# Kernel optimization log

Hardware: AMD Instinct MI355X
Metric: run time of the kernel (lower is better)

The kernel has to match this reference:

```python
import jax, jax.numpy as jnp
import numpy as np
from jax import lax

DIM = 64
HEADS = 4
B, Q, V = 8, 128, 128


def _modrelu(z, b):
    m = jnp.abs(z)
    return z * (jax.nn.relu(m + b) / (m + 1e-5))


def _eunn_unitary(h, th1, ph1, th2, ph2, om):
    # tunable-style EUNN, capacity 2: even-pair rotations, odd-pair rotations, diagonal phase
    d = h.shape[-1]
    # layer 1: pairs (0,1),(2,3),...
    hp = h.reshape(*h.shape[:-1], d // 2, 2)
    a, b = hp[..., 0], hp[..., 1]
    c1, s1, e1 = jnp.cos(th1), jnp.sin(th1), jnp.exp(1j * ph1)
    h = jnp.stack([e1 * (c1 * a - s1 * b), s1 * a + c1 * b], -1).reshape(h.shape)
    # layer 2: pairs (1,2),(3,4),...,(d-3,d-2); endpoints pass through
    mid = h[..., 1:d - 1].reshape(*h.shape[:-1], d // 2 - 1, 2)
    a, b = mid[..., 0], mid[..., 1]
    c2, s2, e2 = jnp.cos(th2), jnp.sin(th2), jnp.exp(1j * ph2)
    mid2 = jnp.stack([e2 * (c2 * a - s2 * b), s2 * a + c2 * b], -1).reshape(*h.shape[:-1], d - 2)
    h = jnp.concatenate([h[..., :1], mid2, h[..., d - 1:]], -1)
    return h * jnp.exp(1j * om)


def _forward(queries, values, U_re, U_im, bias, theta1, phi1, theta2, phi2, omega, W_dense, b_dense):
    Bq, Qq, d = queries.shape
    Vv = values.shape[1]
    # quadratic (query, value) expansion -> [B*Q, V, 2d]
    dq = jnp.broadcast_to(queries[:, :, None, :], (Bq, Qq, Vv, d))
    dv = jnp.broadcast_to(values[:, None, :, :], (Bq, Qq, Vv, d))
    x = jnp.concatenate([dq, dv], -1).reshape(Bq * Qq, Vv, 2 * d)
    U = (U_re + 1j * U_im)  # [H, 2d, d] complex input kernel per head
    Ux = jnp.einsum('nvi,hij->hvnj', x.astype(jnp.complex64), U)  # [H, V, N, d]

    def run_head(Ux_h, t1, p1, t2, p2, om, bh):
        def step(h, u):
            h2 = _modrelu(_eunn_unitary(h, t1, p1, t2, p2, om) + u, bh)
            return h2, None
        h0 = jnp.zeros(Ux_h.shape[1:], dtype=jnp.complex64)  # [N, d]
        hT, _ = lax.scan(step, h0, Ux_h)
        return hT  # final state, as Keras RNN with return_sequences=False

    outs = jax.vmap(run_head)(Ux, theta1, phi1, theta2, phi2, omega, bias)  # [H, N, d]
    acc = jnp.real(outs).transpose(1, 0, 2).reshape(Bq * Qq, HEADS * d)
    y = acc @ W_dense + b_dense
    return y.reshape(Bq, Qq, d)


def setup_inputs() -> dict:
    key = jax.random.key(0)
    ks = jax.random.split(key, 12)
    pi = np.pi
    return {
        'queries': jax.random.normal(ks[0], (B, Q, DIM), jnp.float32),
        'values': jax.random.normal(ks[1], (B, V, DIM), jnp.float32),
        'U_re': jax.random.normal(ks[2], (HEADS, 2 * DIM, DIM), jnp.float32) * (1.0 / np.sqrt(2 * DIM)),
        'U_im': jax.random.normal(ks[3], (HEADS, 2 * DIM, DIM), jnp.float32) * (1.0 / np.sqrt(2 * DIM)),
        'bias': jax.random.normal(ks[4], (HEADS, DIM), jnp.float32) * 0.01,
        'theta1': jax.random.uniform(ks[5], (HEADS, DIM // 2), jnp.float32, -pi, pi),
        'phi1': jax.random.uniform(ks[6], (HEADS, DIM // 2), jnp.float32, -pi, pi),
        'theta2': jax.random.uniform(ks[7], (HEADS, DIM // 2 - 1), jnp.float32, -pi, pi),
        'phi2': jax.random.uniform(ks[8], (HEADS, DIM // 2 - 1), jnp.float32, -pi, pi),
        'omega': jax.random.uniform(ks[9], (HEADS, DIM), jnp.float32, -pi, pi),
        'W_dense': jax.random.normal(ks[10], (HEADS * DIM, DIM), jnp.float32) * (1.0 / np.sqrt(HEADS * DIM)),
        'b_dense': jnp.zeros((DIM,), jnp.float32),
    }


def reference(queries, values, U_re, U_im, bias, theta1, phi1, theta2, phi2, omega, W_dense, b_dense):
    return _forward(queries, values, U_re, U_im, bias, theta1, phi1, theta2, phi2, omega, W_dense, b_dense)
```

## Files before the change

kernel.cpp:

```cpp
#include <hip/hip_runtime.h>
#include <math.h>

#define DIM 64
#define HEADS 4
#define BB 8
#define QQ 128
#define VV 128
#define NN (BB*QQ)

typedef float f2 __attribute__((ext_vector_type(2)));

template <int CTRL>
__device__ __forceinline__ float dppf(float x) {
    return __int_as_float(__builtin_amdgcn_update_dpp(
        0, __float_as_int(x), CTRL, 0xF, 0xF, true));
}
#define SWAP1 0xB1
#define WSHR1 0x138
#define WSHL1 0x130

__global__ __launch_bounds__(256) void k_av(const float* __restrict__ values,
                                            const float* __restrict__ U_re,
                                            const float* __restrict__ U_im,
                                            f2* __restrict__ Av) {
    int tid = blockIdx.x * blockDim.x + threadIdx.x;
    int w = tid >> 6;
    int j = tid & 63;
    int h = w >> 9;
    int r0 = (w & 511) << 1;
    const float* vrow = values + r0 * DIM;
    const float* ur = U_re + (h * 2 * DIM + DIM) * DIM + j;
    const float* ui = U_im + (h * 2 * DIM + DIM) * DIM + j;
    f2 a0 = 0.f, a1 = 0.f;
    #pragma unroll 8
    for (int i = 0; i < DIM; ++i) {
        f2 u; u.x = ur[i * DIM]; u.y = ui[i * DIM];
        a0 += vrow[i] * u;
        a1 += vrow[DIM + i] * u;
    }
    f2* out = Av + (h * 1024 + r0) * DIM + j;
    out[0] = a0; out[DIM] = a1;
}

__global__ __launch_bounds__(256, 4) void k_rnn_dense(
        const float* __restrict__ queries,
        const float* __restrict__ U_re,
        const float* __restrict__ U_im,
        const float* __restrict__ bias,
        const float* __restrict__ theta1,
        const float* __restrict__ phi1,
        const float* __restrict__ theta2,
        const float* __restrict__ phi2,
        const float* __restrict__ omega,
        const f2* __restrict__ Av,
        const float* __restrict__ W_dense,
        const float* __restrict__ b_dense,
        float* __restrict__ y) {
    int n = blockIdx.x;
    int t = threadIdx.x;
    int h = t >> 6;
    int j = t & 63;
    int b = n >> 7;

    int k1 = j >> 1;
    float th1 = theta1[h * 32 + k1], ph1 = phi1[h * 32 + k1];
    float C1 = cosf(th1), s1v = sinf(th1);
    float S1, E1r, E1i;
    if ((j & 1) == 0) { S1 = -s1v; E1r = cosf(ph1); E1i = sinf(ph1); }
    else              { S1 =  s1v; E1r = 1.f;       E1i = 0.f;       }

    float C2, SL, SR, p2r, p2i;
    if (j == 0 || j == 63) {
        C2 = 1.f; SL = 0.f; SR = 0.f; p2r = 1.f; p2i = 0.f;
    } else {
        int k2 = (j - 1) >> 1;
        float th2 = theta2[h * 31 + k2], ph2 = phi2[h * 31 + k2];
        float c2 = cosf(th2), s2 = sinf(th2);
        if (j & 1) { C2 = c2; SL = -s2; SR = 0.f; p2r = cosf(ph2); p2i = sinf(ph2); }
        else       { C2 = c2; SR =  s2; SL = 0.f; p2r = 1.f;       p2i = 0.f;       }
    }
    float om = omega[h * 64 + j];
    float eor = cosf(om), eoi = sinf(om);
    float PHr = p2r * eor - p2i * eoi;
    float PHi = p2r * eoi + p2i * eor;
    float bj = bias[h * 64 + j];

    const float* qrow = queries + n * DIM;
    const float* ur = U_re + (h * 2 * DIM) * DIM + j;
    const float* ui = U_im + (h * 2 * DIM) * DIM + j;
    float uqr = 0.f, uqi = 0.f;
    #pragma unroll 8
    for (int i = 0; i < DIM; ++i) {
        float a = qrow[i];
        uqr = fmaf(a, ur[i * DIM], uqr);
        uqi = fmaf(a, ui[i * DIM], uqi);
    }

    float hr = 0.f, hi = 0.f;
    auto step = [&](f2 av) {
        float uvr = uqr + av.x;
        float uvi = uqi + av.y;
        float pr = dppf<SWAP1>(hr), pi = dppf<SWAP1>(hi);
        float tpr = fmaf(C1, hr, S1 * pr);
        float tpi = fmaf(C1, hi, S1 * pi);
        float Tr = fmaf(E1r, tpr, -E1i * tpi);
        float Ti = fmaf(E1r, tpi,  E1i * tpr);
        float Lr = dppf<WSHL1>(Tr), Li = dppf<WSHL1>(Ti);
        float Rr = dppf<WSHR1>(Tr), Ri = dppf<WSHR1>(Ti);
        float spr = fmaf(C2, Tr, fmaf(SL, Lr, SR * Rr));
        float spi = fmaf(C2, Ti, fmaf(SL, Li, SR * Ri));
        float zr = fmaf(PHr, spr, fmaf(-PHi, spi, uvr));
        float zi = fmaf(PHr, spi, fmaf( PHi, spr, uvi));
        float q2 = fmaf(zr, zr, fmaf(zi, zi, 1e-10f));
        float rs = __builtin_amdgcn_rsqf(q2);
        float sc = fmaxf(fmaf(bj, rs, 1.f), 0.f);
        hr = zr * sc; hi = zi * sc;
    };

    const f2* p = Av + (h * 1024 + b * 128) * DIM + j;

    f2 buf[8], nxt[8];
    #pragma unroll
    for (int k = 0; k < 8; ++k) buf[k] = p[k * DIM];

    for (int vb = 0; vb < VV; vb += 8) {
        const f2* pn = p + ((vb < VV - 8) ? 8 * DIM : 0);
        #pragma unroll
        for (int k = 0; k < 8; ++k) nxt[k] = pn[k * DIM];
        p = pn;
        #pragma unroll
        for (int k = 0; k < 8; ++k) step(buf[k]);
        #pragma unroll
        for (int k = 0; k < 8; ++k) buf[k] = nxt[k];
    }

    __shared__ float s_acc[HEADS * DIM];
    __shared__ float s_part[256];
    s_acc[h * 64 + j] = hr;
    __syncthreads();

    {
        int qq = t >> 6, jj = t & 63;
        const float* Wp = W_dense + (qq * 64) * DIM + jj;
        const float* ap = &s_acc[qq * 64];
        float part = 0.f;
        #pragma unroll 8
        for (int k = 0; k < 64; ++k)
            part = fmaf(ap[k], Wp[k * DIM], part);
        s_part[t] = part;
    }
    __syncthreads();
    if (t < 64) {
        y[n * DIM + t] = b_dense[t] + s_part[t] + s_part[64 + t]
                       + s_part[128 + t] + s_part[192 + t];
    }
}

extern "C" void kernel_launch(void* const* d_in, const int* in_sizes, int n_in,
                              void* d_out, int out_size, void* d_ws, size_t ws_size,
                              hipStream_t stream) {
    const float* queries = (const float*)d_in[0];
    const float* values  = (const float*)d_in[1];
    const float* U_re    = (const float*)d_in[2];
    const float* U_im    = (const float*)d_in[3];
    const float* bias    = (const float*)d_in[4];
    const float* theta1  = (const float*)d_in[5];
    const float* phi1    = (const float*)d_in[6];
    const float* theta2  = (const float*)d_in[7];
    const float* phi2    = (const float*)d_in[8];
    const float* omega   = (const float*)d_in[9];
    const float* W_dense = (const float*)d_in[10];
    const float* b_dense = (const float*)d_in[11];
    float* y = (float*)d_out;

    f2* Av = (f2*)d_ws;

    k_av<<<512, 256, 0, stream>>>(values, U_re, U_im, Av);
    k_rnn_dense<<<1024, 256, 0, stream>>>(queries, U_re, U_im, bias, theta1,
                                          phi1, theta2, phi2, omega, Av,
                                          W_dense, b_dense, y);
}
```

Before: 113.3 us.

## Process two query rows per block to interleave independent RNN chains

```diff
diff --git a/kernel.cpp b/kernel.cpp
--- a/kernel.cpp
+++ b/kernel.cpp
@@ -9,6 +9,7 @@
 #define NN (BB*QQ)
 
 typedef float f2 __attribute__((ext_vector_type(2)));
+typedef float f4 __attribute__((ext_vector_type(4)));
 
 template <int CTRL>
 __device__ __forceinline__ float dppf(float x) {
@@ -22,12 +23,13 @@
 __global__ __launch_bounds__(256) void k_av(const float* __restrict__ values,
                                             const float* __restrict__ U_re,
                                             const float* __restrict__ U_im,
-                                            f2* __restrict__ Av) {
+                                            f4* __restrict__ AvP) {
     int tid = blockIdx.x * blockDim.x + threadIdx.x;
     int w = tid >> 6;
     int j = tid & 63;
     int h = w >> 9;
-    int r0 = (w & 511) << 1;
+    int rp = w & 511;
+    int r0 = rp << 1;
     const float* vrow = values + r0 * DIM;
     const float* ur = U_re + (h * 2 * DIM + DIM) * DIM + j;
     const float* ui = U_im + (h * 2 * DIM + DIM) * DIM + j;
@@ -38,11 +40,11 @@
         a0 += vrow[i] * u;
         a1 += vrow[DIM + i] * u;
     }
-    f2* out = Av + (h * 1024 + r0) * DIM + j;
-    out[0] = a0; out[DIM] = a1;
-}
-
-__global__ __launch_bounds__(256, 4) void k_rnn_dense(
+    f4 o; o.x = a0.x; o.y = a0.y; o.z = a1.x; o.w = a1.y;
+    AvP[(h * 512 + rp) * 64 + j] = o;
+}
+
+__global__ __launch_bounds__(256, 2) void k_rnn_dense(
         const float* __restrict__ queries,
         const float* __restrict__ U_re,
         const float* __restrict__ U_im,
@@ -52,15 +54,16 @@
         const float* __restrict__ theta2,
         const float* __restrict__ phi2,
         const float* __restrict__ omega,
-        const f2* __restrict__ Av,
+        const f4* __restrict__ AvP,
         const float* __restrict__ W_dense,
         const float* __restrict__ b_dense,
         float* __restrict__ y) {
-    int n = blockIdx.x;
+    int m = blockIdx.x;
+    int n0 = m << 1;
     int t = threadIdx.x;
     int h = t >> 6;
     int j = t & 63;
-    int b = n >> 7;
+    int b = n0 >> 7;
 
     int k1 = j >> 1;
     float th1 = theta1[h * 32 + k1], ph1 = phi1[h * 32 + k1];
@@ -85,74 +88,97 @@
     float PHi = p2r * eoi + p2i * eor;
     float bj = bias[h * 64 + j];
 
-    const float* qrow = queries + n * DIM;
+    const float* q0 = queries + n0 * DIM;
+    const float* q1 = q0 + DIM;
     const float* ur = U_re + (h * 2 * DIM) * DIM + j;
     const float* ui = U_im + (h * 2 * DIM) * DIM + j;
-    float uqr = 0.f, uqi = 0.f;
+    float uq0r = 0.f, uq0i = 0.f, uq1r = 0.f, uq1i = 0.f;
     #pragma unroll 8
     for (int i = 0; i < DIM; ++i) {
-        float a = qrow[i];
-        uqr = fmaf(a, ur[i * DIM], uqr);
-        uqi = fmaf(a, ui[i * DIM], uqi);
-    }
-
-    float hr = 0.f, hi = 0.f;
-    auto step = [&](f2 av) {
-        float uvr = uqr + av.x;
-        float uvi = uqi + av.y;
-        float pr = dppf<SWAP1>(hr), pi = dppf<SWAP1>(hi);
-        float tpr = fmaf(C1, hr, S1 * pr);
-        float tpi = fmaf(C1, hi, S1 * pi);
-        float Tr = fmaf(E1r, tpr, -E1i * tpi);
-        float Ti = fmaf(E1r, tpi,  E1i * tpr);
-        float Lr = dppf<WSHL1>(Tr), Li = dppf<WSHL1>(Ti);
-        float Rr = dppf<WSHR1>(Tr), Ri = dppf<WSHR1>(Ti);
-        float spr = fmaf(C2, Tr, fmaf(SL, Lr, SR * Rr));
-        float spi = fmaf(C2, Ti, fmaf(SL, Li, SR * Ri));
-        float zr = fmaf(PHr, spr, fmaf(-PHi, spi, uvr));
-        float zi = fmaf(PHr, spi, fmaf( PHi, spr, uvi));
-        float q2 = fmaf(zr, zr, fmaf(zi, zi, 1e-10f));
-        float rs = __builtin_amdgcn_rsqf(q2);
-        float sc = fmaxf(fmaf(bj, rs, 1.f), 0.f);
-        hr = zr * sc; hi = zi * sc;
+        float u_r = ur[i * DIM], u_i = ui[i * DIM];
+        float a0 = q0[i], a1 = q1[i];
+        uq0r = fmaf(a0, u_r, uq0r);  uq0i = fmaf(a0, u_i, uq0i);
+        uq1r = fmaf(a1, u_r, uq1r);  uq1i = fmaf(a1, u_i, uq1i);
+    }
+
+    float h0r = 0.f, h0i = 0.f, h1r = 0.f, h1i = 0.f;
+    auto step = [&](float avr, float avi) {
+        float uv0r = uq0r + avr, uv0i = uq0i + avi;
+        float uv1r = uq1r + avr, uv1i = uq1i + avi;
+        float p0r = dppf<SWAP1>(h0r), p0i = dppf<SWAP1>(h0i);
+        float p1r = dppf<SWAP1>(h1r), p1i = dppf<SWAP1>(h1i);
+        float tp0r = fmaf(C1, h0r, S1 * p0r), tp0i = fmaf(C1, h0i, S1 * p0i);
+        float tp1r = fmaf(C1, h1r, S1 * p1r), tp1i = fmaf(C1, h1i, S1 * p1i);
+        float T0r = fmaf(E1r, tp0r, -E1i * tp0i), T0i = fmaf(E1r, tp0i, E1i * tp0r);
+        float T1r = fmaf(E1r, tp1r, -E1i * tp1i), T1i = fmaf(E1r, tp1i, E1i * tp1r);
+        float L0r = dppf<WSHL1>(T0r), L0i = dppf<WSHL1>(T0i);
+        float L1r = dppf<WSHL1>(T1r), L1i = dppf<WSHL1>(T1i);
+        float R0r = dppf<WSHR1>(T0r), R0i = dppf<WSHR1>(T0i);
+        float R1r = dppf<WSHR1>(T1r), R1i = dppf<WSHR1>(T1i);
+        float sp0r = fmaf(C2, T0r, fmaf(SL, L0r, SR * R0r));
+        float sp0i = fmaf(C2, T0i, fmaf(SL, L0i, SR * R0i));
+        float sp1r = fmaf(C2, T1r, fmaf(SL, L1r, SR * R1r));
+        float sp1i = fmaf(C2, T1i, fmaf(SL, L1i, SR * R1i));
+        float z0r = fmaf(PHr, sp0r, fmaf(-PHi, sp0i, uv0r));
+        float z0i = fmaf(PHr, sp0i, fmaf( PHi, sp0r, uv0i));
+        float z1r = fmaf(PHr, sp1r, fmaf(-PHi, sp1i, uv1r));
+        float z1i = fmaf(PHr, sp1i, fmaf( PHi, sp1r, uv1i));
+        float q20 = fmaf(z0r, z0r, fmaf(z0i, z0i, 1e-10f));
+        float q21 = fmaf(z1r, z1r, fmaf(z1i, z1i, 1e-10f));
+        float rs0 = __builtin_amdgcn_rsqf(q20);
+        float rs1 = __builtin_amdgcn_rsqf(q21);
+        float sc0 = fmaxf(fmaf(bj, rs0, 1.f), 0.f);
+        float sc1 = fmaxf(fmaf(bj, rs1, 1.f), 0.f);
+        h0r = z0r * sc0; h0i = z0i * sc0;
+        h1r = z1r * sc1; h1i = z1i * sc1;
     };
 
-    const f2* p = Av + (h * 1024 + b * 128) * DIM + j;
-
-    f2 buf[8], nxt[8];
+    const f4* p = AvP + (h * 512 + b * 64) * 64 + j;
+    f4 buf[4], nxt[4];
     #pragma unroll
-    for (int k = 0; k < 8; ++k) buf[k] = p[k * DIM];
-
-    for (int vb = 0; vb < VV; vb += 8) {
-        const f2* pn = p + ((vb < VV - 8) ? 8 * DIM : 0);
+    for (int k = 0; k < 4; ++k) buf[k] = p[k * 64];
+
+    for (int w = 0; w < 16; ++w) {
+        const f4* pn = p + ((w < 15) ? 4 * 64 : 0);
         #pragma unroll
-        for (int k = 0; k < 8; ++k) nxt[k] = pn[k * DIM];
+        for (int k = 0; k < 4; ++k) nxt[k] = pn[k * 64];
         p = pn;
         #pragma unroll
-        for (int k = 0; k < 8; ++k) step(buf[k]);
+        for (int k = 0; k < 4; ++k) {
+            step(buf[k].x, buf[k].y);
+            step(buf[k].z, buf[k].w);
+        }
         #pragma unroll
-        for (int k = 0; k < 8; ++k) buf[k] = nxt[k];
-    }
-
-    __shared__ float s_acc[HEADS * DIM];
-    __shared__ float s_part[256];
-    s_acc[h * 64 + j] = hr;
+        for (int k = 0; k < 4; ++k) buf[k] = nxt[k];
+    }
+
+    __shared__ float s_acc[2][HEADS * DIM];
+    __shared__ float s_part[2][256];
+    s_acc[0][h * 64 + j] = h0r;
+    s_acc[1][h * 64 + j] = h1r;
     __syncthreads();
 
     {
         int qq = t >> 6, jj = t & 63;
         const float* Wp = W_dense + (qq * 64) * DIM + jj;
-        const float* ap = &s_acc[qq * 64];
-        float part = 0.f;
+        const float* a0 = &s_acc[0][qq * 64];
+        const float* a1 = &s_acc[1][qq * 64];
+        float part0 = 0.f, part1 = 0.f;
         #pragma unroll 8
-        for (int k = 0; k < 64; ++k)
-            part = fmaf(ap[k], Wp[k * DIM], part);
-        s_part[t] = part;
+        for (int k = 0; k < 64; ++k) {
+            float wv = Wp[k * DIM];
+            part0 = fmaf(a0[k], wv, part0);
+            part1 = fmaf(a1[k], wv, part1);
+        }
+        s_part[0][t] = part0;
+        s_part[1][t] = part1;
     }
     __syncthreads();
-    if (t < 64) {
-        y[n * DIM + t] = b_dense[t] + s_part[t] + s_part[64 + t]
-                       + s_part[128 + t] + s_part[192 + t];
+    if (t < 128) {
+        int r = t >> 6, c = t & 63;
+        y[(n0 + r) * DIM + c] = b_dense[c]
+            + s_part[r][c] + s_part[r][64 + c]
+            + s_part[r][128 + c] + s_part[r][192 + c];
     }
 }
 
@@ -173,10 +199,10 @@
     const float* b_dense = (const float*)d_in[11];
     float* y = (float*)d_out;
 
-    f2* Av = (f2*)d_ws;
-
-    k_av<<<512, 256, 0, stream>>>(values, U_re, U_im, Av);
-    k_rnn_dense<<<1024, 256, 0, stream>>>(queries, U_re, U_im, bias, theta1,
-                                          phi1, theta2, phi2, omega, Av,
-                                          W_dense, b_dense, y);
-}
+    f4* AvP = (f4*)d_ws;
+
+    k_av<<<512, 256, 0, stream>>>(values, U_re, U_im, AvP);
+    k_rnn_dense<<<512, 256, 0, stream>>>(queries, U_re, U_im, bias, theta1,
+                                         phi1, theta2, phi2, omega, AvP,
+                                         W_dense, b_dense, y);
+}
```

New measurement: 112.7 us. Within noise of the previous version (-0.6%).

## Precompute EUNN coefficients once, pack Av as float4, use packed f2 math

Applied to the files above, without the earlier changes.

```diff
diff --git a/kernel.cpp b/kernel.cpp
--- a/kernel.cpp
+++ b/kernel.cpp
@@ -9,6 +9,7 @@
 #define NN (BB*QQ)
 
 typedef float f2 __attribute__((ext_vector_type(2)));
+typedef float f4 __attribute__((ext_vector_type(4)));
 
 template <int CTRL>
 __device__ __forceinline__ float dppf(float x) {
@@ -19,15 +20,27 @@
 #define WSHR1 0x138
 #define WSHL1 0x130
 
+__device__ __forceinline__ f2 b2(float s) { f2 r; r.x = s; r.y = s; return r; }
+#define SW(v) __builtin_shufflevector((v), (v), 1, 0)
+#define FMA2(a, b, c) __builtin_elementwise_fma((a), (b), (c))
+
 __global__ __launch_bounds__(256) void k_av(const float* __restrict__ values,
                                             const float* __restrict__ U_re,
                                             const float* __restrict__ U_im,
-                                            f2* __restrict__ Av) {
+                                            const float* __restrict__ bias,
+                                            const float* __restrict__ theta1,
+                                            const float* __restrict__ phi1,
+                                            const float* __restrict__ theta2,
+                                            const float* __restrict__ phi2,
+                                            const float* __restrict__ omega,
+                                            f4* __restrict__ AvP,
+                                            float* __restrict__ Coef) {
     int tid = blockIdx.x * blockDim.x + threadIdx.x;
     int w = tid >> 6;
     int j = tid & 63;
     int h = w >> 9;
-    int r0 = (w & 511) << 1;
+    int rp = w & 511;
+    int r0 = rp << 1;
     const float* vrow = values + r0 * DIM;
     const float* ur = U_re + (h * 2 * DIM + DIM) * DIM + j;
     const float* ui = U_im + (h * 2 * DIM + DIM) * DIM + j;
@@ -38,21 +51,51 @@
         a0 += vrow[i] * u;
         a1 += vrow[DIM + i] * u;
     }
-    f2* out = Av + (h * 1024 + r0) * DIM + j;
-    out[0] = a0; out[DIM] = a1;
+    f4 o; o.x = a0.x; o.y = a0.y; o.z = a1.x; o.w = a1.y;
+    AvP[(h * 512 + rp) * 64 + j] = o;
+
+    if (blockIdx.x == 0) {
+        int t = threadIdx.x;
+        int hh = t >> 6, jj = t & 63;
+        int k1 = jj >> 1;
+        float th1 = theta1[hh * 32 + k1], ph1 = phi1[hh * 32 + k1];
+        float C1 = cosf(th1), s1v = sinf(th1);
+        float S1, E1r, E1i;
+        if ((jj & 1) == 0) { S1 = -s1v; E1r = cosf(ph1); E1i = sinf(ph1); }
+        else               { S1 =  s1v; E1r = 1.f;       E1i = 0.f;       }
+        float C2, SL, SR, p2r, p2i;
+        if (jj == 0 || jj == 63) {
+            C2 = 1.f; SL = 0.f; SR = 0.f; p2r = 1.f; p2i = 0.f;
+        } else {
+            int k2 = (jj - 1) >> 1;
+            float th2 = theta2[hh * 31 + k2], ph2 = phi2[hh * 31 + k2];
+            float c2 = cosf(th2), s2 = sinf(th2);
+            if (jj & 1) { C2 = c2; SL = -s2; SR = 0.f; p2r = cosf(ph2); p2i = sinf(ph2); }
+            else        { C2 = c2; SR =  s2; SL = 0.f; p2r = 1.f;       p2i = 0.f;      }
+        }
+        float om = omega[hh * 64 + jj];
+        float eor = cosf(om), eoi = sinf(om);
+        float PHr = p2r * eor - p2i * eoi;
+        float PHi = p2r * eoi + p2i * eor;
+        Coef[0 * 256 + t] = C1;
+        Coef[1 * 256 + t] = S1;
+        Coef[2 * 256 + t] = E1r;
+        Coef[3 * 256 + t] = E1i;
+        Coef[4 * 256 + t] = C2;
+        Coef[5 * 256 + t] = SL;
+        Coef[6 * 256 + t] = SR;
+        Coef[7 * 256 + t] = PHr;
+        Coef[8 * 256 + t] = PHi;
+        Coef[9 * 256 + t] = bias[hh * 64 + jj];
+    }
 }
 
 __global__ __launch_bounds__(256, 4) void k_rnn_dense(
         const float* __restrict__ queries,
         const float* __restrict__ U_re,
         const float* __restrict__ U_im,
-        const float* __restrict__ bias,
-        const float* __restrict__ theta1,
-        const float* __restrict__ phi1,
-        const float* __restrict__ theta2,
-        const float* __restrict__ phi2,
-        const float* __restrict__ omega,
-        const f2* __restrict__ Av,
+        const float* __restrict__ Coef,
+        const f4* __restrict__ AvP,
         const float* __restrict__ W_dense,
         const float* __restrict__ b_dense,
         float* __restrict__ y) {
@@ -62,81 +105,72 @@
     int j = t & 63;
     int b = n >> 7;
 
-    int k1 = j >> 1;
-    float th1 = theta1[h * 32 + k1], ph1 = phi1[h * 32 + k1];
-    float C1 = cosf(th1), s1v = sinf(th1);
-    float S1, E1r, E1i;
-    if ((j & 1) == 0) { S1 = -s1v; E1r = cosf(ph1); E1i = sinf(ph1); }
-    else              { S1 =  s1v; E1r = 1.f;       E1i = 0.f;       }
-
-    float C2, SL, SR, p2r, p2i;
-    if (j == 0 || j == 63) {
-        C2 = 1.f; SL = 0.f; SR = 0.f; p2r = 1.f; p2i = 0.f;
-    } else {
-        int k2 = (j - 1) >> 1;
-        float th2 = theta2[h * 31 + k2], ph2 = phi2[h * 31 + k2];
-        float c2 = cosf(th2), s2 = sinf(th2);
-        if (j & 1) { C2 = c2; SL = -s2; SR = 0.f; p2r = cosf(ph2); p2i = sinf(ph2); }
-        else       { C2 = c2; SR =  s2; SL = 0.f; p2r = 1.f;       p2i = 0.f;       }
-    }
-    float om = omega[h * 64 + j];
-    float eor = cosf(om), eoi = sinf(om);
-    float PHr = p2r * eor - p2i * eoi;
-    float PHi = p2r * eoi + p2i * eor;
-    float bj = bias[h * 64 + j];
-
-    const float* qrow = queries + n * DIM;
+    float C1  = Coef[0 * 256 + t];
+    float S1  = Coef[1 * 256 + t];
+    float E1r = Coef[2 * 256 + t];
+    float E1i = Coef[3 * 256 + t];
+    float C2  = Coef[4 * 256 + t];
+    float SL  = Coef[5 * 256 + t];
+    float SR  = Coef[6 * 256 + t];
+    float PHr = Coef[7 * 256 + t];
+    float PHi = Coef[8 * 256 + t];
+    float bj  = Coef[9 * 256 + t];
+
+    f2 C1p = b2(C1), S1p = b2(S1), E1rp = b2(E1r);
+    f2 E1in; E1in.x = -E1i; E1in.y = E1i;
+    f2 C2p = b2(C2), SLp = b2(SL), SRp = b2(SR), PHrp = b2(PHr);
+    f2 PHin; PHin.x = -PHi; PHin.y = PHi;
+
+    const float* q0 = queries + n * DIM;
     const float* ur = U_re + (h * 2 * DIM) * DIM + j;
     const float* ui = U_im + (h * 2 * DIM) * DIM + j;
-    float uqr = 0.f, uqi = 0.f;
+    f2 uq = 0.f;
     #pragma unroll 8
     for (int i = 0; i < DIM; ++i) {
-        float a = qrow[i];
-        uqr = fmaf(a, ur[i * DIM], uqr);
-        uqi = fmaf(a, ui[i * DIM], uqi);
-    }
-
-    float hr = 0.f, hi = 0.f;
+        f2 u; u.x = ur[i * DIM]; u.y = ui[i * DIM];
+        uq = FMA2(b2(q0[i]), u, uq);
+    }
+
+    f2 hS = 0.f;
     auto step = [&](f2 av) {
-        float uvr = uqr + av.x;
-        float uvi = uqi + av.y;
-        float pr = dppf<SWAP1>(hr), pi = dppf<SWAP1>(hi);
-        float tpr = fmaf(C1, hr, S1 * pr);
-        float tpi = fmaf(C1, hi, S1 * pi);
-        float Tr = fmaf(E1r, tpr, -E1i * tpi);
-        float Ti = fmaf(E1r, tpi,  E1i * tpr);
-        float Lr = dppf<WSHL1>(Tr), Li = dppf<WSHL1>(Ti);
-        float Rr = dppf<WSHR1>(Tr), Ri = dppf<WSHR1>(Ti);
-        float spr = fmaf(C2, Tr, fmaf(SL, Lr, SR * Rr));
-        float spi = fmaf(C2, Ti, fmaf(SL, Li, SR * Ri));
-        float zr = fmaf(PHr, spr, fmaf(-PHi, spi, uvr));
-        float zi = fmaf(PHr, spi, fmaf( PHi, spr, uvi));
-        float q2 = fmaf(zr, zr, fmaf(zi, zi, 1e-10f));
+        f2 uv = uq + av;
+        f2 p; p.x = dppf<SWAP1>(hS.x); p.y = dppf<SWAP1>(hS.y);
+        f2 tp = FMA2(C1p, hS, S1p * p);
+        f2 T  = FMA2(E1rp, tp, E1in * SW(tp));
+        f2 L; L.x = dppf<WSHL1>(T.x); L.y = dppf<WSHL1>(T.y);
+        f2 R; R.x = dppf<WSHR1>(T.x); R.y = dppf<WSHR1>(T.y);
+        f2 sp = FMA2(C2p, T, FMA2(SLp, L, SRp * R));
+        f2 z  = FMA2(PHrp, sp, FMA2(PHin, SW(sp), uv));
+        float q2 = fmaf(z.x, z.x, fmaf(z.y, z.y, 1e-10f));
         float rs = __builtin_amdgcn_rsqf(q2);
         float sc = fmaxf(fmaf(bj, rs, 1.f), 0.f);
-        hr = zr * sc; hi = zi * sc;
+        hS = z * b2(sc);
     };
 
-    const f2* p = Av + (h * 1024 + b * 128) * DIM + j;
-
-    f2 buf[8], nxt[8];
+    const f4* p = AvP + (h * 512 + b * 64) * 64 + j;
+    f4 buf[4], nxt[4];
     #pragma unroll
-    for (int k = 0; k < 8; ++k) buf[k] = p[k * DIM];
-
-    for (int vb = 0; vb < VV; vb += 8) {
-        const f2* pn = p + ((vb < VV - 8) ? 8 * DIM : 0);
+    for (int k = 0; k < 4; ++k) buf[k] = p[k * 64];
+
+    for (int w = 0; w < 16; ++w) {
+        const f4* pn = p + ((w < 15) ? 4 * 64 : 0);
         #pragma unroll
-        for (int k = 0; k < 8; ++k) nxt[k] = pn[k * DIM];
+        for (int k = 0; k < 4; ++k) nxt[k] = pn[k * 64];
         p = pn;
         #pragma unroll
-        for (int k = 0; k < 8; ++k) step(buf[k]);
+        for (int k = 0; k < 4; ++k) {
+            f2 a; a.x = buf[k].x; a.y = buf[k].y;
+            step(a);
+            f2 c; c.x = buf[k].z; c.y = buf[k].w;
+            step(c);
+        }
         #pragma unroll
-        for (int k = 0; k < 8; ++k) buf[k] = nxt[k];
+        for (int k = 0; k < 4; ++k) buf[k] = nxt[k];
     }
 
     __shared__ float s_acc[HEADS * DIM];
     __shared__ float s_part[256];
-    s_acc[h * 64 + j] = hr;
+    s_acc[h * 64 + j] = hS.x;
     __syncthreads();
 
     {
@@ -173,10 +207,11 @@
     const float* b_dense = (const float*)d_in[11];
     float* y = (float*)d_out;
 
-    f2* Av = (f2*)d_ws;
-
-    k_av<<<512, 256, 0, stream>>>(values, U_re, U_im, Av);
-    k_rnn_dense<<<1024, 256, 0, stream>>>(queries, U_re, U_im, bias, theta1,
-                                          phi1, theta2, phi2, omega, Av,
+    f4* AvP = (f4*)d_ws;
+    float* Coef = (float*)((char*)d_ws + HEADS * 512 * 64 * sizeof(f4));
+
+    k_av<<<512, 256, 0, stream>>>(values, U_re, U_im, bias, theta1, phi1,
+                                  theta2, phi2, omega, AvP, Coef);
+    k_rnn_dense<<<1024, 256, 0, stream>>>(queries, U_re, U_im, Coef, AvP,
                                           W_dense, b_dense, y);
 }
```

New measurement: 115.9 us. +2.3%, slower.
